# Performance work log

Measured on AMD Instinct MI355X. Metric: run time of the kernel, lower is better.

## Reference

```python
import jax, jax.numpy as jnp
import numpy as np

B, NG, NM, E, K, D = 1, 65536, 8192, 262144, 32, 128
EPS = 1e-5


def layernorm(x, g, b):
    mu = jnp.mean(x, axis=-1, keepdims=True)
    var = jnp.mean(jnp.square(x - mu), axis=-1, keepdims=True)
    return (x - mu) * jax.lax.rsqrt(var + EPS) * g + b


def mlp(x, W, g, b):
    # Linear (no bias) -> tanh -> LayerNorm, matching MLP module
    return layernorm(jnp.tanh(x @ W), g, b)


def setup_inputs() -> dict:
    key = jax.random.key(0)
    ks = jax.random.split(key, 16)
    inp = {
        "grid_mesh_bond_embedding": jax.random.normal(ks[0], (B, E, D), jnp.float32),
        "grid_rect_embedding": jax.random.normal(ks[1], (B, NG, D), jnp.float32),
        "mesh_node_embedding": jax.random.normal(ks[2], (B, NM, D), jnp.float32),
        "edge_id2pair": jnp.stack(
            [jax.random.randint(ks[3], (E,), 0, NG),
             jax.random.randint(ks[4], (E,), 0, NM)], axis=1),  # [E,2] int
        "edge_id_of_node": jax.random.randint(ks[5], (NM, K), 0, E),  # [NM,K] int
        "edge_coef": jax.random.uniform(ks[6], (NM, K, 1), jnp.float32),
        # MLP_G2M_GM2E: Linear(3D -> D), LayerNorm(D)
        "W_gm2e": jax.random.normal(ks[7], (3 * D, D), jnp.float32) / np.sqrt(3 * D),
        "g_gm2e": jnp.ones((D,), jnp.float32),
        "b_gm2e": jnp.zeros((D,), jnp.float32),
        # MLP_G2M_E2M: Linear(2D -> D), LayerNorm(D)
        "W_e2m": jax.random.normal(ks[8], (2 * D, D), jnp.float32) / np.sqrt(2 * D),
        "g_e2m": jnp.ones((D,), jnp.float32),
        "b_e2m": jnp.zeros((D,), jnp.float32),
        # MLP_G2M_G2G: Linear(D -> D), LayerNorm(D)
        "W_g2g": jax.random.normal(ks[9], (D, D), jnp.float32) / np.sqrt(D),
        "g_g2g": jnp.ones((D,), jnp.float32),
        "b_g2g": jnp.zeros((D,), jnp.float32),
    }
    return inp


def reference(grid_mesh_bond_embedding, grid_rect_embedding, mesh_node_embedding,
              edge_id2pair, edge_id_of_node, edge_coef,
              W_gm2e, g_gm2e, b_gm2e, W_e2m, g_e2m, b_e2m, W_g2g, g_g2g, b_g2g):
    # Edge update: gather rect/node endpoints, concat, MLP -> [B,E,D]
    rect_src = grid_rect_embedding[:, edge_id2pair[:, 0]]  # [B,E,D]
    node_dst = mesh_node_embedding[:, edge_id2pair[:, 1]]  # [B,E,D]
    edge_in = jnp.concatenate([grid_mesh_bond_embedding, rect_src, node_dst], axis=-1)
    delta_edge = mlp(edge_in, W_gm2e, g_gm2e, b_gm2e)  # [B,E,D]

    # Node update: gather K edges per mesh node, coef-weighted mean over K
    gathered = delta_edge[:, edge_id_of_node]  # [B,NM,K,D]
    agg = jnp.mean(gathered * edge_coef, axis=-2)  # [B,NM,D]
    delta_node = mlp(jnp.concatenate([mesh_node_embedding, agg], axis=-1), W_e2m, g_e2m, b_e2m)

    # Grid rect self-update
    delta_rect = mlp(grid_rect_embedding, W_g2g, g_g2g, b_g2g)

    return (grid_mesh_bond_embedding + delta_edge,
            grid_rect_embedding + delta_rect,
            mesh_node_embedding + delta_node)
```

## Files before the change

kernel.cpp:

```cpp
#include <hip/hip_runtime.h>


typedef __bf16 bf16x8 __attribute__((ext_vector_type(8)));
typedef __bf16 bf16x4 __attribute__((ext_vector_type(4)));
typedef float f32x4 __attribute__((ext_vector_type(4)));
typedef unsigned int u32x4 __attribute__((ext_vector_type(4)));

#define E_CNT 262144
#define NG_CNT 65536
#define NM_CNT 8192

#define WF_A 0
#define WF_B 16384
#define WF_C 32768
#define WF_3 49152
#define WF_2 65536
#define WF_TOT 98304

__device__ __forceinline__ float fast_tanh(float x) {
  float e = __expf(2.f * x);
  return 1.f - 2.f / (1.f + e);
}

__global__ __launch_bounds__(256) void convert_w_kernel(
    const float* __restrict__ W1, const float* __restrict__ W2,
    const float* __restrict__ W3, __bf16* __restrict__ WF) {
  const int cid = blockIdx.x * 256 + threadIdx.x;
  if (cid >= 12288) return;
  const float* src;
  __bf16* dst;
  int local;
  if (cid < 2048) { src = W1; local = cid; dst = WF + WF_A; }
  else if (cid < 4096) { src = W1 + 128 * 128; local = cid - 2048; dst = WF + WF_B; }
  else if (cid < 6144) { src = W1 + 256 * 128; local = cid - 4096; dst = WF + WF_C; }
  else if (cid < 8192) { src = W3; local = cid - 6144; dst = WF + WF_3; }
  else { src = W2; local = cid - 8192; dst = WF + WF_2; }
  const int lane6 = local & 63, cx = lane6 & 15, qq = lane6 >> 4;
  const int kkn = local >> 6, kk = kkn >> 3, nn = kkn & 7;
  const int k0 = kk * 32 + qq * 8, col = nn * 16 + cx;
  bf16x8 v;
#pragma unroll
  for (int j = 0; j < 8; ++j) v[j] = (__bf16)src[(k0 + j) * 128 + col];
  *(bf16x8*)(dst + local * 8) = v;
}

__device__ __forceinline__ void stage_copy(const __bf16* __restrict__ wf,
                                           __bf16* wt, int nelems) {
  const int n16 = nelems >> 3;
  for (int i = threadIdx.x; i < n16; i += blockDim.x)
    *(u32x4*)(wt + i * 8) = *(const u32x4*)(wf + i * 8);
}

template <bool STORE_D, bool NT>
__device__ __forceinline__ void mlp_epilogue(f32x4* acc, const f32x4* R,
                                             const float* gvec,
                                             const float* bvec, int q,
                                             float* op, __bf16* dp) {
  float s1 = 0.f, s2 = 0.f;
#pragma unroll
  for (int n = 0; n < 8; ++n)
#pragma unroll
    for (int j = 0; j < 4; ++j) {
      float v = fast_tanh(acc[n][j]);
      acc[n][j] = v;
      s1 += v;
      s2 += v * v;
    }
  s1 += __shfl_xor(s1, 16, 64);
  s2 += __shfl_xor(s2, 16, 64);
  s1 += __shfl_xor(s1, 32, 64);
  s2 += __shfl_xor(s2, 32, 64);
  const float mu = s1 * (1.f / 128.f);
  const float rs = rsqrtf(s2 * (1.f / 128.f) - mu * mu + 1e-5f);
#pragma unroll
  for (int n = 0; n < 8; ++n) {
    const f32x4 G = *(const f32x4*)(gvec + n * 16 + q * 4);
    const f32x4 Bv = *(const f32x4*)(bvec + n * 16 + q * 4);
    f32x4 o;
    bf16x4 db;
#pragma unroll
    for (int j = 0; j < 4; ++j) {
      const float d = (acc[n][j] - mu) * rs * G[j] + Bv[j];
      o[j] = R[n][j] + d;
      db[j] = (__bf16)d;
    }
    if (NT)
      __builtin_nontemporal_store(o, (f32x4*)(op + n * 16 + q * 4));
    else
      *(f32x4*)(op + n * 16 + q * 4) = o;
    if (STORE_D) *(bf16x4*)(dp + n * 16 + q * 4) = db;
  }
}

template <bool STORE_D>
__global__ __launch_bounds__(256, 4) void edge_kernel(
    const float* __restrict__ gm, const int* __restrict__ pair,
    const __bf16* __restrict__ P1, const __bf16* __restrict__ P2,
    const __bf16* __restrict__ WF, const float* __restrict__ gvec,
    const float* __restrict__ bvec, float* __restrict__ out,
    __bf16* __restrict__ delta_out) {
  __shared__ __bf16 wt[16384];
  stage_copy(WF, wt, 16384);
  __syncthreads();
  const int tid = threadIdx.x, lane = tid & 63, wid = tid >> 6;
  const int r = lane & 15, q = lane >> 4;
  const __bf16* wl = wt + lane * 8;
  const int row = ((blockIdx.x * 4 + wid) << 4) + r;

  const int2 sd = *(const int2*)(pair + 2 * (size_t)row);
  const float* pa = gm + (size_t)row * 128;
  f32x4 F[4][2];
#pragma unroll
  for (int kk = 0; kk < 4; ++kk) {
    F[kk][0] = *(const f32x4*)(pa + kk * 32 + q * 8);
    F[kk][1] = *(const f32x4*)(pa + kk * 32 + q * 8 + 4);
  }
  bf16x4 pg1[8], pg2[8];
  {
    const __bf16* p1 = P1 + (size_t)sd.x * 128 + q * 4;
    const __bf16* p2 = P2 + (size_t)sd.y * 128 + q * 4;
#pragma unroll
    for (int n = 0; n < 8; ++n) {
      pg1[n] = *(const bf16x4*)(p1 + n * 16);
      pg2[n] = *(const bf16x4*)(p2 + n * 16);
    }
  }

  bf16x8 ab[4];
#pragma unroll
  for (int kk = 0; kk < 4; ++kk)
#pragma unroll
    for (int j = 0; j < 4; ++j) {
      ab[kk][j] = (__bf16)F[kk][0][j];
      ab[kk][4 + j] = (__bf16)F[kk][1][j];
    }
  f32x4 acc[8] = {};
#pragma unroll
  for (int kk = 0; kk < 4; ++kk)
#pragma unroll
    for (int n = 0; n < 8; ++n)
      acc[n] = __builtin_amdgcn_mfma_f32_16x16x32_bf16(
          *(const bf16x8*)(wl + (kk * 8 + n) * 512), ab[kk], acc[n], 0, 0, 0);
#pragma unroll
  for (int n = 0; n < 8; ++n)
#pragma unroll
    for (int j = 0; j < 4; ++j)
      acc[n][j] += (float)pg1[n][j] + (float)pg2[n][j];

  f32x4 R[8];
#pragma unroll
  for (int n = 0; n < 8; ++n) R[n] = *(const f32x4*)(pa + n * 16 + q * 4);

  mlp_epilogue<STORE_D, false>(acc, R, gvec, bvec, q, out + (size_t)row * 128,
                               STORE_D ? delta_out + (size_t)row * 128 : nullptr);
}

__global__ __launch_bounds__(256) void rect_fused_kernel(
    const float* __restrict__ rect, const __bf16* __restrict__ WFb,
    const __bf16* __restrict__ WF3, const float* __restrict__ gvec,
    const float* __restrict__ bvec, float* __restrict__ out1,
    __bf16* __restrict__ P1) {
  const int tid = threadIdx.x, lane = tid & 63, wid = tid >> 6;
  const int r = lane & 15, q = lane >> 4;
  const __bf16* wlb = WFb + lane * 8;
  const __bf16* wl3 = WF3 + lane * 8;
  const int row = ((blockIdx.x * 4 + wid) << 4) + r;
  const float* pa = rect + (size_t)row * 128;
  f32x4 F[4][2];
#pragma unroll
  for (int kk = 0; kk < 4; ++kk) {
    F[kk][0] = *(const f32x4*)(pa + kk * 32 + q * 8);
    F[kk][1] = *(const f32x4*)(pa + kk * 32 + q * 8 + 4);
  }
  f32x4 R[8];
#pragma unroll
  for (int n = 0; n < 8; ++n) R[n] = *(const f32x4*)(pa + n * 16 + q * 4);
  bf16x8 ab[4];
#pragma unroll
  for (int kk = 0; kk < 4; ++kk)
#pragma unroll
    for (int j = 0; j < 4; ++j) {
      ab[kk][j] = (__bf16)F[kk][0][j];
      ab[kk][4 + j] = (__bf16)F[kk][1][j];
    }
  f32x4 acc[8] = {};
#pragma unroll
  for (int kk = 0; kk < 4; ++kk)
#pragma unroll
    for (int n = 0; n < 8; ++n)
      acc[n] = __builtin_amdgcn_mfma_f32_16x16x32_bf16(
          *(const bf16x8*)(wlb + (kk * 8 + n) * 512), ab[kk], acc[n], 0, 0, 0);
  __bf16* pp = P1 + (size_t)row * 128;
#pragma unroll
  for (int n = 0; n < 8; ++n) {
    bf16x4 o;
#pragma unroll
    for (int j = 0; j < 4; ++j) o[j] = (__bf16)acc[n][j];
    *(bf16x4*)(pp + n * 16 + q * 4) = o;
  }
  f32x4 acc2[8] = {};
#pragma unroll
  for (int kk = 0; kk < 4; ++kk)
#pragma unroll
    for (int n = 0; n < 8; ++n)
      acc2[n] = __builtin_amdgcn_mfma_f32_16x16x32_bf16(
          *(const bf16x8*)(wl3 + (kk * 8 + n) * 512), ab[kk], acc2[n], 0, 0, 0);
  mlp_epilogue<false, true>(acc2, R, gvec, bvec, q, out1 + (size_t)row * 128,
                            nullptr);
}

__global__ __launch_bounds__(256) void mlp128_kernel(
    const float* __restrict__ A, const __bf16* __restrict__ WFx,
    const float* __restrict__ gvec, const float* __restrict__ bvec,
    float* __restrict__ out, int M) {
  const int tid = threadIdx.x, lane = tid & 63, wid = tid >> 6;
  const int r = lane & 15, q = lane >> 4;
  const __bf16* wl = WFx + lane * 8;
  const int t = blockIdx.x * 4 + wid;
  if (t >= (M >> 4)) return;
  const int row = (t << 4) + r;
  const float* pa = A + (size_t)row * 128;
  f32x4 F[4][2];
#pragma unroll
  for (int kk = 0; kk < 4; ++kk) {
    F[kk][0] = *(const f32x4*)(pa + kk * 32 + q * 8);
    F[kk][1] = *(const f32x4*)(pa + kk * 32 + q * 8 + 4);
  }
  bf16x8 ab[4];
#pragma unroll
  for (int kk = 0; kk < 4; ++kk)
#pragma unroll
    for (int j = 0; j < 4; ++j) {
      ab[kk][j] = (__bf16)F[kk][0][j];
      ab[kk][4 + j] = (__bf16)F[kk][1][j];
    }
  f32x4 acc[8] = {};
#pragma unroll
  for (int kk = 0; kk < 4; ++kk)
#pragma unroll
    for (int n = 0; n < 8; ++n)
      acc[n] = __builtin_amdgcn_mfma_f32_16x16x32_bf16(
          *(const bf16x8*)(wl + (kk * 8 + n) * 512), ab[kk], acc[n], 0, 0, 0);
  f32x4 R[8];
#pragma unroll
  for (int n = 0; n < 8; ++n) R[n] = *(const f32x4*)(pa + n * 16 + q * 4);
  mlp_epilogue<false, true>(acc, R, gvec, bvec, q, out + (size_t)row * 128,
                            nullptr);
}

__global__ __launch_bounds__(256) void lin_kernel(
    const float* __restrict__ A, const __bf16* __restrict__ WFx,
    __bf16* __restrict__ out, int M) {
  const int tid = threadIdx.x, lane = tid & 63, wid = tid >> 6;
  const int r = lane & 15, q = lane >> 4;
  const __bf16* wl = WFx + lane * 8;
  const int t = blockIdx.x * 4 + wid;
  if (t >= (M >> 4)) return;
  const int row = (t << 4) + r;
  const float* pa = A + (size_t)row * 128;
  f32x4 F[4][2];
#pragma unroll
  for (int kk = 0; kk < 4; ++kk) {
    F[kk][0] = *(const f32x4*)(pa + kk * 32 + q * 8);
    F[kk][1] = *(const f32x4*)(pa + kk * 32 + q * 8 + 4);
  }
  bf16x8 ab[4];
#pragma unroll
  for (int kk = 0; kk < 4; ++kk)
#pragma unroll
    for (int j = 0; j < 4; ++j) {
      ab[kk][j] = (__bf16)F[kk][0][j];
      ab[kk][4 + j] = (__bf16)F[kk][1][j];
    }
  f32x4 acc[8] = {};
#pragma unroll
  for (int kk = 0; kk < 4; ++kk)
#pragma unroll
    for (int n = 0; n < 8; ++n)
      acc[n] = __builtin_amdgcn_mfma_f32_16x16x32_bf16(
          *(const bf16x8*)(wl + (kk * 8 + n) * 512), ab[kk], acc[n], 0, 0, 0);
  __bf16* po = out + (size_t)row * 128;
#pragma unroll
  for (int n = 0; n < 8; ++n) {
    bf16x4 o;
#pragma unroll
    for (int j = 0; j < 4; ++j) o[j] = (__bf16)acc[n][j];
    *(bf16x4*)(po + n * 16 + q * 4) = o;
  }
}

__global__ __launch_bounds__(256) void node_kernel(
    const __bf16* __restrict__ Ab, const __bf16* __restrict__ WF2,
    const float* __restrict__ gvec, const float* __restrict__ bvec,
    const float* __restrict__ resid, float* __restrict__ out, int M) {
  const int tid = threadIdx.x, lane = tid & 63, wid = tid >> 6;
  const int r = lane & 15, q = lane >> 4;
  const __bf16* wl = WF2 + lane * 8;
  const int t = blockIdx.x * 4 + wid;
  if (t >= (M >> 4)) return;
  const int row = (t << 4) + r;
  const __bf16* pb = Ab + (size_t)row * 256 + q * 8;
  bf16x8 ab[8];
#pragma unroll
  for (int kk = 0; kk < 8; ++kk) ab[kk] = *(const bf16x8*)(pb + kk * 32);
  f32x4 R[8];
#pragma unroll
  for (int n = 0; n < 8; ++n)
    R[n] = *(const f32x4*)(resid + (size_t)row * 128 + n * 16 + q * 4);
  f32x4 acc[8] = {};
#pragma unroll
  for (int kk = 0; kk < 8; ++kk)
#pragma unroll
    for (int n = 0; n < 8; ++n)
      acc[n] = __builtin_amdgcn_mfma_f32_16x16x32_bf16(
          *(const bf16x8*)(wl + (kk * 8 + n) * 512), ab[kk], acc[n], 0, 0, 0);
  mlp_epilogue<false, true>(acc, R, gvec, bvec, q, out + (size_t)row * 128,
                            nullptr);
}

template <bool FROM_WS>
__global__ __launch_bounds__(256) void agg_kernel(
    const __bf16* __restrict__ dws, const float* __restrict__ out0,
    const float* __restrict__ gm, const float* __restrict__ mesh,
    const int* __restrict__ eid, const float* __restrict__ coef,
    __bf16* __restrict__ x2) {
  __shared__ int eid_s[512];
  __shared__ float cf_s[512];
  const int t = threadIdx.x;
  const int n0 = blockIdx.x * 16;
  for (int i = t; i < 512; i += 256) {
    eid_s[i] = eid[n0 * 32 + i];
    cf_s[i] = coef[n0 * 32 + i];
  }
  __syncthreads();
  const int rl = t >> 4;
  const int d8 = (t & 15) * 8;
  const int row = n0 + rl;
  float acc[8] = {0, 0, 0, 0, 0, 0, 0, 0};
#pragma unroll 8
  for (int k = 0; k < 32; ++k) {
    const int e = eid_s[rl * 32 + k];
    const float cf = cf_s[rl * 32 + k];
    if (FROM_WS) {
      bf16x8 v = *(const bf16x8*)(dws + (size_t)e * 128 + d8);
#pragma unroll
      for (int j = 0; j < 8; ++j) acc[j] += cf * (float)v[j];
    } else {
      const float* po = out0 + (size_t)e * 128 + d8;
      const float* pg = gm + (size_t)e * 128 + d8;
      f32x4 o0 = *(const f32x4*)po, o1 = *(const f32x4*)(po + 4);
      f32x4 g0 = *(const f32x4*)pg, g1 = *(const f32x4*)(pg + 4);
#pragma unroll
      for (int j = 0; j < 4; ++j) {
        acc[j] += cf * (o0[j] - g0[j]);
        acc[4 + j] += cf * (o1[j] - g1[j]);
      }
    }
  }
  const float* pm = mesh + (size_t)row * 128 + d8;
  f32x4 m0 = *(const f32x4*)pm, m1 = *(const f32x4*)(pm + 4);
  bf16x8 mv, av;
#pragma unroll
  for (int j = 0; j < 4; ++j) {
    mv[j] = (__bf16)m0[j];
    mv[4 + j] = (__bf16)m1[j];
  }
#pragma unroll
  for (int j = 0; j < 8; ++j) av[j] = (__bf16)(acc[j] * (1.0f / 32.0f));
  *(bf16x8*)(x2 + (size_t)row * 256 + d8) = mv;
  *(bf16x8*)(x2 + (size_t)row * 256 + 128 + d8) = av;
}

extern "C" void kernel_launch(void* const* d_in, const int* in_sizes, int n_in,
                              void* d_out, int out_size, void* d_ws,
                              size_t ws_size, hipStream_t stream) {
  const float* gm = (const float*)d_in[0];
  const float* rect = (const float*)d_in[1];
  const float* mesh = (const float*)d_in[2];
  const int* pair = (const int*)d_in[3];
  const int* eid = (const int*)d_in[4];
  const float* coef = (const float*)d_in[5];
  const float* W1 = (const float*)d_in[6];
  const float* g1 = (const float*)d_in[7];
  const float* b1 = (const float*)d_in[8];
  const float* W2 = (const float*)d_in[9];
  const float* g2 = (const float*)d_in[10];
  const float* b2 = (const float*)d_in[11];
  const float* W3 = (const float*)d_in[12];
  const float* g3 = (const float*)d_in[13];
  const float* b3 = (const float*)d_in[14];

  float* out0 = (float*)d_out;
  float* out1 = out0 + (size_t)E_CNT * 128;
  float* out2 = out1 + (size_t)NG_CNT * 128;

  const size_t wfBytes = (size_t)WF_TOT * 2;
  const size_t wfoff = (ws_size - wfBytes) & ~(size_t)63;
  __bf16* WF = (__bf16*)((char*)d_ws + wfoff);

  const size_t deltaE = (size_t)E_CNT * 128;
  const size_t x2E = (size_t)NM_CNT * 256;
  const size_t p1E = (size_t)NG_CNT * 128;
  const bool fastD = wfoff >= (deltaE + x2E) * 2;
  const bool fastP = wfoff >= (deltaE + x2E + p1E) * 2;

  __bf16* delta = (__bf16*)d_ws;
  __bf16* x2 = fastD ? delta + deltaE : (__bf16*)d_ws;
  __bf16* P1ws = delta + deltaE + x2E;
  __bf16* P2 = (__bf16*)out2;

  convert_w_kernel<<<48, 256, 0, stream>>>(W1, W2, W3, WF);

  const __bf16* P1;
  if (fastP) {
    rect_fused_kernel<<<1024, 256, 0, stream>>>(rect, WF + WF_B, WF + WF_3, g3,
                                                b3, out1, P1ws);
    P1 = P1ws;
  } else {
    lin_kernel<<<1024, 256, 0, stream>>>(rect, WF + WF_B, (__bf16*)out1,
                                         NG_CNT);
    P1 = (const __bf16*)out1;
  }
  lin_kernel<<<128, 256, 0, stream>>>(mesh, WF + WF_C, P2, NM_CNT);

  if (fastD) {
    edge_kernel<true><<<4096, 256, 0, stream>>>(gm, pair, P1, P2, WF + WF_A,
                                                g1, b1, out0, delta);
    agg_kernel<true><<<512, 256, 0, stream>>>(delta, nullptr, nullptr, mesh,
                                              eid, coef, x2);
  } else {
    edge_kernel<false><<<4096, 256, 0, stream>>>(gm, pair, P1, P2, WF + WF_A,
                                                 g1, b1, out0, nullptr);
    agg_kernel<false><<<512, 256, 0, stream>>>(nullptr, out0, gm, mesh, eid,
                                               coef, x2);
  }
  if (!fastP) {
    mlp128_kernel<<<1024, 256, 0, stream>>>(rect, WF + WF_3, g3, b3, out1,
                                            NG_CNT);
  }
  node_kernel<<<128, 256, 0, stream>>>(x2, WF + WF_2, g2, b2, mesh, out2,
                                       NM_CNT);
}
```

Baseline: 188.6 us.

## Split edge gather into separate pre-summed, MFMA-layout buffer kernel

Adds a gather kernel that reads the rect and mesh projections for each edge with coalesced 16-byte loads, sums them, and writes a bf16 buffer already laid out for the MFMA accumulator. A new dense edge kernel then reads that buffer contiguously instead of doing scattered 8-byte gathers inside the matmul kernel. The aim is to improve memory access efficiency and latency hiding. The cost is an extra kernel launch plus writing and rereading a 64 MB intermediate, and the path only runs when the workspace is large enough.

```diff
diff --git a/kernel.cpp b/kernel.cpp
--- a/kernel.cpp
+++ b/kernel.cpp
@@ -44,6 +44,27 @@
   *(bf16x8*)(dst + local * 8) = v;
 }
 
+__global__ __launch_bounds__(256) void gather_pg_kernel(
+    const int* __restrict__ pair, const __bf16* __restrict__ P1,
+    const __bf16* __restrict__ P2, __bf16* __restrict__ PG) {
+  const int t = threadIdx.x;
+  const int rl = t >> 4, d = t & 15;
+  const int e = blockIdx.x * 16 + rl;
+  const int2 sd = *(const int2*)(pair + 2 * (size_t)e);
+  bf16x8 a = *(const bf16x8*)(P1 + (size_t)sd.x * 128 + d * 8);
+  bf16x8 b = *(const bf16x8*)(P2 + (size_t)sd.y * 128 + d * 8);
+  bf16x4 lo, hi;
+#pragma unroll
+  for (int j = 0; j < 4; ++j) {
+    lo[j] = (__bf16)((float)a[j] + (float)b[j]);
+    hi[j] = (__bf16)((float)a[4 + j] + (float)b[4 + j]);
+  }
+  const int n = d >> 1, q0 = (d & 1) * 2;
+  __bf16* base = PG + (size_t)blockIdx.x * 2048;
+  *(bf16x4*)(base + (q0 * 16 + rl) * 32 + n * 4) = lo;
+  *(bf16x4*)(base + ((q0 + 1) * 16 + rl) * 32 + n * 4) = hi;
+}
+
 __device__ __forceinline__ void stage_copy(const __bf16* __restrict__ wf,
                                            __bf16* wt, int nelems) {
   const int n16 = nelems >> 3;
@@ -90,6 +111,62 @@
       *(f32x4*)(op + n * 16 + q * 4) = o;
     if (STORE_D) *(bf16x4*)(dp + n * 16 + q * 4) = db;
   }
+}
+
+template <bool STORE_D>
+__global__ __launch_bounds__(256, 4) void edge_dense_kernel(
+    const float* __restrict__ gm, const __bf16* __restrict__ PG,
+    const __bf16* __restrict__ WF, const float* __restrict__ gvec,
+    const float* __restrict__ bvec, float* __restrict__ out,
+    __bf16* __restrict__ delta_out) {
+  __shared__ __bf16 wt[16384];
+  stage_copy(WF, wt, 16384);
+  __syncthreads();
+  const int tid = threadIdx.x, lane = tid & 63, wid = tid >> 6;
+  const int r = lane & 15, q = lane >> 4;
+  const __bf16* wl = wt + lane * 8;
+  const int t = blockIdx.x * 4 + wid;
+  const int row = (t << 4) + r;
+  const float* pa = gm + (size_t)row * 128;
+
+  f32x4 F[4][2];
+#pragma unroll
+  for (int kk = 0; kk < 4; ++kk) {
+    F[kk][0] = *(const f32x4*)(pa + kk * 32 + q * 8);
+    F[kk][1] = *(const f32x4*)(pa + kk * 32 + q * 8 + 4);
+  }
+  const __bf16* pgp = PG + (size_t)t * 2048 + lane * 32;
+  bf16x8 pgv[4];
+#pragma unroll
+  for (int i = 0; i < 4; ++i) pgv[i] = *(const bf16x8*)(pgp + i * 8);
+
+  bf16x8 ab[4];
+#pragma unroll
+  for (int kk = 0; kk < 4; ++kk)
+#pragma unroll
+    for (int j = 0; j < 4; ++j) {
+      ab[kk][j] = (__bf16)F[kk][0][j];
+      ab[kk][4 + j] = (__bf16)F[kk][1][j];
+    }
+  f32x4 acc[8] = {};
+#pragma unroll
+  for (int kk = 0; kk < 4; ++kk)
+#pragma unroll
+    for (int n = 0; n < 8; ++n)
+      acc[n] = __builtin_amdgcn_mfma_f32_16x16x32_bf16(
+          *(const bf16x8*)(wl + (kk * 8 + n) * 512), ab[kk], acc[n], 0, 0, 0);
+#pragma unroll
+  for (int n = 0; n < 8; ++n)
+#pragma unroll
+    for (int j = 0; j < 4; ++j)
+      acc[n][j] += (float)pgv[n >> 1][(n & 1) * 4 + j];
+
+  f32x4 R[8];
+#pragma unroll
+  for (int n = 0; n < 8; ++n) R[n] = *(const f32x4*)(pa + n * 16 + q * 4);
+
+  mlp_epilogue<STORE_D, false>(acc, R, gvec, bvec, q, out + (size_t)row * 128,
+                               STORE_D ? delta_out + (size_t)row * 128 : nullptr);
 }
 
 template <bool STORE_D>
@@ -106,7 +183,6 @@
   const int r = lane & 15, q = lane >> 4;
   const __bf16* wl = wt + lane * 8;
   const int row = ((blockIdx.x * 4 + wid) << 4) + r;
-
   const int2 sd = *(const int2*)(pair + 2 * (size_t)row);
   const float* pa = gm + (size_t)row * 128;
   f32x4 F[4][2];
@@ -125,7 +201,6 @@
       pg2[n] = *(const bf16x4*)(p2 + n * 16);
     }
   }
-
   bf16x8 ab[4];
 #pragma unroll
   for (int kk = 0; kk < 4; ++kk)
@@ -146,11 +221,9 @@
 #pragma unroll
     for (int j = 0; j < 4; ++j)
       acc[n][j] += (float)pg1[n][j] + (float)pg2[n][j];
-
   f32x4 R[8];
 #pragma unroll
   for (int n = 0; n < 8; ++n) R[n] = *(const f32x4*)(pa + n * 16 + q * 4);
-
   mlp_epilogue<STORE_D, false>(acc, R, gvec, bvec, q, out + (size_t)row * 128,
                                STORE_D ? delta_out + (size_t)row * 128 : nullptr);
 }
@@ -401,12 +474,15 @@
   const size_t deltaE = (size_t)E_CNT * 128;
   const size_t x2E = (size_t)NM_CNT * 256;
   const size_t p1E = (size_t)NG_CNT * 128;
+  const size_t pgE = (size_t)E_CNT * 128;
   const bool fastD = wfoff >= (deltaE + x2E) * 2;
   const bool fastP = wfoff >= (deltaE + x2E + p1E) * 2;
+  const bool fastG = wfoff >= (deltaE + x2E + p1E + pgE) * 2;
 
   __bf16* delta = (__bf16*)d_ws;
   __bf16* x2 = fastD ? delta + deltaE : (__bf16*)d_ws;
   __bf16* P1ws = delta + deltaE + x2E;
+  __bf16* PGws = P1ws + p1E;
   __bf16* P2 = (__bf16*)out2;
 
   convert_w_kernel<<<48, 256, 0, stream>>>(W1, W2, W3, WF);
@@ -423,7 +499,13 @@
   }
   lin_kernel<<<128, 256, 0, stream>>>(mesh, WF + WF_C, P2, NM_CNT);
 
-  if (fastD) {
+  if (fastG) {
+    gather_pg_kernel<<<E_CNT / 16, 256, 0, stream>>>(pair, P1, P2, PGws);
+    edge_dense_kernel<true><<<4096, 256, 0, stream>>>(gm, PGws, WF + WF_A, g1,
+                                                      b1, out0, delta);
+    agg_kernel<true><<<512, 256, 0, stream>>>(delta, nullptr, nullptr, mesh,
+                                              eid, coef, x2);
+  } else if (fastD) {
     edge_kernel<true><<<4096, 256, 0, stream>>>(gm, pair, P1, P2, WF + WF_A,
                                                 g1, b1, out0, delta);
     agg_kernel<true><<<512, 256, 0, stream>>>(delta, nullptr, nullptr, mesh,
```

New measurement: 205.2 us. 1.09x slower.
